# Performance work log

Measured on AMD Instinct MI355X. Metric: run time of the kernel, lower is better.

The kernel has to match this reference:

```python
import jax, jax.numpy as jnp
import numpy as np

N = 20000      # nodes
E = 320000     # edges (avg degree 16)
IN = 512       # input feature dim
HID = 64       # hidden_dim
NH = 8         # n_heads
NC = 20        # n_classes
NG = 64        # graphs in batch
EPS = 1e-5     # batchnorm eps


def setup_inputs() -> dict:
    key = jax.random.key(0)
    ks = jax.random.split(key, 32)
    rn = lambda k, shape, s=0.05: (jax.random.normal(k, shape, jnp.float32) * s)
    inp = {
        "x": rn(ks[0], (N, IN), 1.0),
        "src": jax.random.randint(ks[1], (E,), 0, N),
        "dst": jax.random.randint(ks[2], (E,), 0, N),
        "graph_ids": jnp.sort(jax.random.randint(ks[3], (N,), 0, NG)),
        "n_graphs": NG,
        # encoder
        "W_enc": rn(ks[4], (IN, HID)), "b_enc": jnp.zeros((HID,), jnp.float32),
        # GAT layer 0
        "fc_W0": rn(ks[5], (HID, NH * HID)),
        "attn_l0": rn(ks[6], (NH, HID)), "attn_r0": rn(ks[7], (NH, HID)),
        "res_W0": rn(ks[8], (HID, NH * HID)),
        "bias0": jnp.zeros((NH * HID,), jnp.float32),
        "dp_W0": rn(ks[9], (NH * HID, HID)), "dp_b0": jnp.zeros((HID,), jnp.float32),
        # GAT layer 1
        "fc_W1": rn(ks[10], (HID, NH * HID)),
        "attn_l1": rn(ks[11], (NH, HID)), "attn_r1": rn(ks[12], (NH, HID)),
        "res_W1": rn(ks[13], (HID, NH * HID)),
        "bias1": jnp.zeros((NH * HID,), jnp.float32),
        "dp_W1": rn(ks[14], (NH * HID, HID)), "dp_b1": jnp.zeros((HID,), jnp.float32),
        # batchnorm affine
        "gamma": jnp.ones((2 * HID,), jnp.float32), "beta": jnp.zeros((2 * HID,), jnp.float32),
        # global attention pooling gate
        "gate_W": rn(ks[15], (2 * HID, 1)), "gate_b": jnp.zeros((1,), jnp.float32),
        # classifier
        "cls_W": rn(ks[16], (2 * HID, NC)), "cls_b": jnp.zeros((NC,), jnp.float32),
    }
    return inp


def gat_conv(h, fc_W, attn_l, attn_r, res_W, bias, src, dst, n_nodes):
    # DGL GATConv: fc -> per-head scalar scores -> edge softmax over incoming
    # edges -> weighted sum -> residual + bias -> leaky_relu activation.
    nh, d = attn_l.shape
    feat = (h @ fc_W).reshape(n_nodes, nh, d)              # [N,H,D]
    el = jnp.sum(feat * attn_l[None], axis=-1)             # [N,H]
    er = jnp.sum(feat * attn_r[None], axis=-1)             # [N,H]
    e = jax.nn.leaky_relu(el[src] + er[dst], 0.2)          # [E,H]
    m = jax.ops.segment_max(e, dst, num_segments=n_nodes)  # segment softmax
    ex = jnp.exp(e - m[dst])
    denom = jax.ops.segment_sum(ex, dst, num_segments=n_nodes)
    a = ex / denom[dst]                                    # [E,H]
    msg = feat[src] * a[:, :, None]                        # [E,H,D]  (dominant)
    rst = jax.ops.segment_sum(msg, dst, num_segments=n_nodes)  # [N,H,D]
    rst = rst + (h @ res_W).reshape(n_nodes, nh, d) + bias.reshape(nh, d)
    return jax.nn.leaky_relu(rst, 0.01)  # F.leaky_relu default slope


def reference(x, W_enc, b_enc,
              fc_W0, attn_l0, attn_r0, res_W0, bias0, dp_W0, dp_b0,
              fc_W1, attn_l1, attn_r1, res_W1, bias1, dp_W1, dp_b1,
              gamma, beta, gate_W, gate_b, cls_W, cls_b,
              src, dst, graph_ids, n_graphs):
    n_nodes = x.shape[0]
    he = x @ W_enc + b_enc                                  # encoder [N,HID]
    h = he
    h = gat_conv(h, fc_W0, attn_l0, attn_r0, res_W0, bias0, src, dst, n_nodes)
    h = h.reshape(n_nodes, -1) @ dp_W0 + dp_b0              # down_proj 0
    h = gat_conv(h, fc_W1, attn_l1, attn_r1, res_W1, bias1, src, dst, n_nodes)
    h = h.reshape(n_nodes, -1) @ dp_W1 + dp_b1              # down_proj 1
    hg = jnp.concatenate([h, he], axis=1)                   # [N,2*HID]
    # BatchNorm1d (training-mode batch stats, biased variance)
    mu = jnp.mean(hg, axis=0)
    var = jnp.var(hg, axis=0)
    hg = (hg - mu) * jax.lax.rsqrt(var + EPS) * gamma + beta
    # GlobalAttentionPooling: per-graph softmax over node gates
    gate = hg @ gate_W + gate_b                             # [N,1]
    gm = jax.ops.segment_max(gate, graph_ids, num_segments=n_graphs)
    ge = jnp.exp(gate - gm[graph_ids])
    gden = jax.ops.segment_sum(ge, graph_ids, num_segments=n_graphs)
    alpha = ge / gden[graph_ids]                            # [N,1]
    readout = jax.ops.segment_sum(alpha * hg, graph_ids, num_segments=n_graphs)
    return readout @ cls_W + cls_b                          # [NG,NC]
```

## Files before the change

### kernel.cpp

```cpp
#include <hip/hip_runtime.h>
#include <hip/hip_bf16.h>

#define MROWS   20000
#define N_EDGES 320000
#define DIN     512
#define HID     64
#define NH      8
#define ND      512
#define NCLS    20
#define NG      64
#define BN_EPS  1e-5f
#define PCH     16
#define BNB     256
#define TPB     128

typedef __hip_bfloat16 bf16;
typedef __attribute__((ext_vector_type(8))) short s16x8;
typedef __attribute__((ext_vector_type(4))) float f32x4;

enum { TF32 = 0, TBF16 = 1, TMODE = 2 };

__device__ __forceinline__ int is_bf16_mode(const void* gamma) {
    return *(const unsigned*)gamma != 0x3F800000u;
}

__device__ __forceinline__ float ld_f32(const void* p, size_t i) { return ((const float*)p)[i]; }
__device__ __forceinline__ float ld_b16(const void* p, size_t i) { return __bfloat162float(((const bf16*)p)[i]); }

template<int T>
__device__ __forceinline__ float ldT(const void* p, size_t i, int bf) {
    if constexpr (T == TF32) return ld_f32(p, i);
    else if constexpr (T == TBF16) return ld_b16(p, i);
    else return bf ? ld_b16(p, i) : ld_f32(p, i);
}
template<int T>
__device__ __forceinline__ void stT(void* p, size_t i, int bf, float v) {
    if constexpr (T == TF32) ((float*)p)[i] = v;
    else if constexpr (T == TBF16) ((bf16*)p)[i] = __float2bfloat16(v);
    else { if (bf) ((bf16*)p)[i] = __float2bfloat16(v); else ((float*)p)[i] = v; }
}

__device__ __forceinline__ float bfbits2f(short s) {
    return __uint_as_float(((unsigned)(unsigned short)s) << 16);
}
__device__ __forceinline__ short f2bfbits(float v) {
    bf16 b = __float2bfloat16(v);
    return *reinterpret_cast<short*>(&b);
}

struct TP { const void* src[7]; bf16* dst[7]; int K[7]; };
__global__ void prep_kernel(TP tp, const void* __restrict__ x, bf16* __restrict__ xb,
                            const void* __restrict__ gamma, int* __restrict__ zero0) {
    int b = blockIdx.x;
    int z = b * 256 + threadIdx.x;
    if (z < 2 * MROWS) zero0[z] = 0;
    const int bf = is_bf16_mode(gamma);
    if (b < 7 * TPB) {
        int id = b / TPB;
        int i = (b - id * TPB) * 256 + threadIdx.x;
        int K = tp.K[id];
        int N = (DIN * HID) / K;
        int n = i / K, k = i - n * K;
        tp.dst[id][i] = __float2bfloat16(ldT<TMODE>(tp.src[id], (size_t)k * N + n, bf));
    } else {
        if (bf) return;
        int i = ((b - 7 * TPB) * 256 + threadIdx.x) * 4;
        if (i >= MROWS * DIN) return;
        float4 v = ((const float4*)x)[i >> 2];
        xb[i + 0] = __float2bfloat16(v.x);
        xb[i + 1] = __float2bfloat16(v.y);
        xb[i + 2] = __float2bfloat16(v.z);
        xb[i + 3] = __float2bfloat16(v.w);
    }
}

__global__ void hist_kernel(const int* __restrict__ keys, int* __restrict__ counts, int n) {
    int i = blockIdx.x * 256 + threadIdx.x;
    if (i < n) atomicAdd(&counts[keys[i]], 1);
}

__global__ __launch_bounds__(1024)
void scan_all_kernel(const int* __restrict__ counts, int* __restrict__ offs,
                     const int* __restrict__ gids, int* __restrict__ goffs) {
    if (threadIdx.x <= NG) {
        int g = threadIdx.x;
        int lo = 0, hi = MROWS;
        while (lo < hi) {
            int mid = (lo + hi) >> 1;
            if (gids[mid] < g) lo = mid + 1; else hi = mid;
        }
        goffs[g] = lo;
    }
    __shared__ int wsum[16];
    __shared__ int carry_s;
    int carry = 0;
    int lane = threadIdx.x & 63, wid = threadIdx.x >> 6;
    const int NCHUNK = (MROWS + 1023) / 1024;
    for (int ch = 0; ch < NCHUNK; ++ch) {
        int i = ch * 1024 + threadIdx.x;
        int v = (i < MROWS) ? counts[i] : 0;
        int s = v;
        #pragma unroll
        for (int o = 1; o < 64; o <<= 1) { int t = __shfl_up(s, o, 64); if (lane >= o) s += t; }
        if (lane == 63) wsum[wid] = s;
        __syncthreads();
        if (wid == 0 && lane < 16) {
            int t = wsum[lane];
            #pragma unroll
            for (int o = 1; o < 16; o <<= 1) { int u = __shfl_up(t, o, 64); if (lane >= o) t += u; }
            wsum[lane] = t;
        }
        __syncthreads();
        int wc = (wid > 0) ? wsum[wid - 1] : 0;
        int incl = s + wc + carry;
        if (i < MROWS) offs[i] = incl - v;
        if (threadIdx.x == 1023) carry_s = incl;
        __syncthreads();
        carry = carry_s;
    }
    if (threadIdx.x == 0) offs[MROWS] = carry;
}

__global__ void scatter_kernel(const int* __restrict__ src, const int* __restrict__ dst,
                               const int* __restrict__ offs, int* __restrict__ cursor,
                               int* __restrict__ src_sorted) {
    int e = blockIdx.x * 256 + threadIdx.x;
    if (e < N_EDGES) {
        int d = dst[e];
        int pos = offs[d] + atomicAdd(&cursor[d], 1);
        src_sorted[pos] = src[e];
    }
}

template<int K, int NB, int NTOT>
__global__ __launch_bounds__(256)
void gemm_mfma(const void* __restrict__ Araw, const bf16* __restrict__ Aconv,
               const bf16* __restrict__ BT, const void* __restrict__ bias,
               bf16* __restrict__ C, const void* __restrict__ gamma) {
    const int bf = is_bf16_mode(gamma);
    const bf16* A = bf ? (const bf16*)Araw : Aconv;
    const int wid  = threadIdx.x >> 6;
    const int lane = threadIdx.x & 63;
    const int quad = lane >> 4;
    const int l16  = lane & 15;
    const int rb = blockIdx.x * 128 + wid * 32;
    const int cb = blockIdx.y * NB;
    constexpr int CT = NB / 16;
    constexpr int KC = K / 32;

    f32x4 acc[2][CT] = {};
    int r0 = rb + l16;       if (r0 >= MROWS) r0 = MROWS - 1;
    int r1 = rb + 16 + l16;  if (r1 >= MROWS) r1 = MROWS - 1;
    const bf16* a0p = A + (size_t)r0 * K + quad * 8;
    const bf16* a1p = A + (size_t)r1 * K + quad * 8;
    const bf16* btp = BT + (size_t)(cb + l16) * K + quad * 8;

    for (int kc = 0; kc < KC; ++kc) {
        s16x8 af0 = *(const s16x8*)(a0p + kc * 32);
        s16x8 af1 = *(const s16x8*)(a1p + kc * 32);
        s16x8 bfr[CT];
        #pragma unroll
        for (int ct = 0; ct < CT; ++ct)
            bfr[ct] = *(const s16x8*)(btp + (size_t)ct * 16 * K + kc * 32);
        #pragma unroll
        for (int ct = 0; ct < CT; ++ct) {
            acc[0][ct] = __builtin_amdgcn_mfma_f32_16x16x32_bf16(af0, bfr[ct], acc[0][ct], 0, 0, 0);
            acc[1][ct] = __builtin_amdgcn_mfma_f32_16x16x32_bf16(af1, bfr[ct], acc[1][ct], 0, 0, 0);
        }
    }
    #pragma unroll
    for (int ct = 0; ct < CT; ++ct) {
        int col = cb + ct * 16 + l16;
        float bb = bias ? ldT<TMODE>(bias, col, bf) : 0.f;
        #pragma unroll
        for (int rt = 0; rt < 2; ++rt) {
            #pragma unroll
            for (int rg = 0; rg < 4; ++rg) {
                int row = rb + rt * 16 + quad * 4 + rg;
                if (row < MROWS)
                    C[(size_t)row * NTOT + col] = __float2bfloat16(acc[rt][ct][rg] + bb);
            }
        }
    }
}

__global__ __launch_bounds__(256)
void gemm_fcres(const bf16* __restrict__ A, const bf16* __restrict__ BT_fc,
                const bf16* __restrict__ BT_res, const void* __restrict__ bias,
                const void* __restrict__ attn_l, const void* __restrict__ attn_r,
                bf16* __restrict__ feat, bf16* __restrict__ rst,
                float* __restrict__ el, float* __restrict__ er,
                const void* __restrict__ gamma) {
    const int bf = is_bf16_mode(gamma);
    const bool isres = blockIdx.y >= 4;
    const int yy = blockIdx.y & 3;
    const bf16* BT = isres ? BT_res : BT_fc;
    bf16* C = isres ? rst : feat;
    const int wid  = threadIdx.x >> 6;
    const int lane = threadIdx.x & 63;
    const int quad = lane >> 4;
    const int l16  = lane & 15;
    const int rb = blockIdx.x * 128 + wid * 32;
    const int cb = yy * 128;
    constexpr int CT = 8;
    constexpr int K  = HID;
    constexpr int KC = K / 32;

    f32x4 acc[2][CT] = {};
    int r0 = rb + l16;       if (r0 >= MROWS) r0 = MROWS - 1;
    int r1 = rb + 16 + l16;  if (r1 >= MROWS) r1 = MROWS - 1;
    const bf16* a0p = A + (size_t)r0 * K + quad * 8;
    const bf16* a1p = A + (size_t)r1 * K + quad * 8;
    const bf16* btp = BT + (size_t)(cb + l16) * K + quad * 8;

    #pragma unroll
    for (int kc = 0; kc < KC; ++kc) {
        s16x8 af0 = *(const s16x8*)(a0p + kc * 32);
        s16x8 af1 = *(const s16x8*)(a1p + kc * 32);
        s16x8 bfr[CT];
        #pragma unroll
        for (int ct = 0; ct < CT; ++ct)
            bfr[ct] = *(const s16x8*)(btp + (size_t)ct * 16 * K + kc * 32);
        #pragma unroll
        for (int ct = 0; ct < CT; ++ct) {
            acc[0][ct] = __builtin_amdgcn_mfma_f32_16x16x32_bf16(af0, bfr[ct], acc[0][ct], 0, 0, 0);
            acc[1][ct] = __builtin_amdgcn_mfma_f32_16x16x32_bf16(af1, bfr[ct], acc[1][ct], 0, 0, 0);
        }
    }
    #pragma unroll
    for (int ct = 0; ct < CT; ++ct) {
        int col = cb + ct * 16 + l16;
        float bb = isres ? ldT<TMODE>(bias, col, bf) : 0.f;
        #pragma unroll
        for (int rt = 0; rt < 2; ++rt) {
            #pragma unroll
            for (int rg = 0; rg < 4; ++rg) {
                int row = rb + rt * 16 + quad * 4 + rg;
                if (row < MROWS)
                    C[(size_t)row * ND + col] = __float2bfloat16(acc[rt][ct][rg] + bb);
            }
        }
    }
    if (!isres) {
        float al[CT], ar[CT];
        #pragma unroll
        for (int ct = 0; ct < CT; ++ct) {
            int col = cb + ct * 16 + l16;
            al[ct] = ldT<TMODE>(attn_l, col, bf);
            ar[ct] = ldT<TMODE>(attn_r, col, bf);
        }
        #pragma unroll
        for (int rt = 0; rt < 2; ++rt) {
            #pragma unroll
            for (int rg = 0; rg < 4; ++rg) {
                float e0 = 0.f, e1 = 0.f, f0 = 0.f, f1 = 0.f;
                #pragma unroll
                for (int ct = 0; ct < 4; ++ct) {
                    e0 += acc[rt][ct][rg] * al[ct];
                    f0 += acc[rt][ct][rg] * ar[ct];
                    e1 += acc[rt][ct + 4][rg] * al[ct + 4];
                    f1 += acc[rt][ct + 4][rg] * ar[ct + 4];
                }
                #pragma unroll
                for (int o = 1; o < 16; o <<= 1) {
                    e0 += __shfl_xor(e0, o, 64);
                    e1 += __shfl_xor(e1, o, 64);
                    f0 += __shfl_xor(f0, o, 64);
                    f1 += __shfl_xor(f1, o, 64);
                }
                int row = rb + rt * 16 + quad * 4 + rg;
                if (row < MROWS) {
                    if (l16 == 0) { el[row * 8 + 2 * yy] = e0;     er[row * 8 + 2 * yy] = f0; }
                    if (l16 == 1) { el[row * 8 + 2 * yy + 1] = e1; er[row * 8 + 2 * yy + 1] = f1; }
                }
            }
        }
    }
}

__global__ __launch_bounds__(256)
void agg_kernel(const bf16* __restrict__ feat, const float* __restrict__ el,
                const float* __restrict__ er, const int* __restrict__ offs,
                const int* __restrict__ srcs, bf16* __restrict__ rst) {
    int gid = blockIdx.x * 256 + threadIdx.x;
    int n = gid >> 6;
    int l = threadIdx.x & 63;
    if (n >= MROWS) return;
    int hh = l >> 3;
    int e0 = __builtin_amdgcn_readfirstlane(offs[n]);
    int e1 = __builtin_amdgcn_readfirstlane(offs[n + 1]);
    float er_h = er[n * 8 + hh];
    float acc[8] = {0.f, 0.f, 0.f, 0.f, 0.f, 0.f, 0.f, 0.f};
    float den = 0.f;
    for (int base = e0; base < e1; base += 64) {
        int cnt = min(64, e1 - base);
        int sv = (base + l < e1) ? srcs[base + l] : 0;
        for (int eb = 0; eb < cnt; eb += 8) {
            int en = cnt - eb;
            s16x8 ff[8];
            float elv[8];
            int lastv = cnt - 1;
            #pragma unroll
            for (int p = 0; p < 8; ++p) {
                int idx = eb + p; if (idx > lastv) idx = lastv;
                int s = __shfl(sv, idx, 64);
                ff[p] = *(const s16x8*)(feat + (size_t)s * ND + l * 8);
                elv[p] = el[s * 8 + hh];
            }
            float ww[8];
            #pragma unroll
            for (int p = 0; p < 8; ++p) {
                float sc = elv[p] + er_h;
                sc = sc > 0.f ? sc : 0.2f * sc;
                ww[p] = __expf(fminf(sc, 30.f));
            }
            if (en < 8) {
                #pragma unroll
                for (int p = 1; p < 8; ++p)
                    if (p >= en) ww[p] = 0.f;
            }
            #pragma unroll
            for (int p = 0; p < 8; ++p) {
                den += ww[p];
                #pragma unroll
                for (int j = 0; j < 8; ++j)
                    acc[j] += bfbits2f(ff[p][j]) * ww[p];
            }
        }
    }
    float inv = (den > 0.f) ? 1.f / den : 0.f;
    s16x8* rp = (s16x8*)(rst + (size_t)n * ND + l * 8);
    s16x8 rr = *rp;
    s16x8 ro;
    #pragma unroll
    for (int j = 0; j < 8; ++j) {
        float r = bfbits2f(rr[j]) + acc[j] * inv;
        r = r > 0.f ? r : 0.01f * r;
        ro[j] = f2bfbits(r);
    }
    *rp = ro;
}

__global__ void bn_part_kernel(const bf16* __restrict__ h2, const bf16* __restrict__ he,
                               float* __restrict__ psum, float* __restrict__ psq) {
    int t = threadIdx.x;
    int b = blockIdx.x;
    int beg = (int)((long)MROWS * b / BNB);
    int end = (int)((long)MROWS * (b + 1) / BNB);
    const bf16* srcb = (t < 64) ? h2 : he;
    int col = t & 63;
    float s = 0.f, s2 = 0.f;
    for (int r = beg; r < end; ++r) {
        float v = __bfloat162float(srcb[(size_t)r * 64 + col]);
        s += v;
        s2 += v * v;
    }
    psum[b * 128 + t] = s;
    psq[b * 128 + t] = s2;
}

__global__ void bn_reduce_kernel(const float* __restrict__ psum, const float* __restrict__ psq,
                                 const void* __restrict__ gamma, const void* __restrict__ beta,
                                 float* __restrict__ scale, float* __restrict__ shift) {
    const int bf = is_bf16_mode(gamma);
    int t = threadIdx.x;
    float s = 0.f, s2 = 0.f;
    for (int b = 0; b < BNB; ++b) { s += psum[b * 128 + t]; s2 += psq[b * 128 + t]; }
    float mu = s * (1.f / MROWS);
    float var = s2 * (1.f / MROWS) - mu * mu;
    float inv = rsqrtf(fmaxf(var, 0.f) + BN_EPS);
    float a = ldT<TMODE>(gamma, t, bf) * inv;
    scale[t] = a;
    shift[t] = ldT<TMODE>(beta, t, bf) - mu * a;
}

__global__ __launch_bounds__(128)
void poolgate_kernel(const bf16* __restrict__ h2, const bf16* __restrict__ he,
                     const float* __restrict__ scale, const float* __restrict__ shift,
                     const void* __restrict__ gate_W, const void* __restrict__ gate_b,
                     const int* __restrict__ goffs,
                     float* __restrict__ pacc, float* __restrict__ pden,
                     const void* __restrict__ gamma) {
    const int bf = is_bf16_mode(gamma);
    int g = blockIdx.x;
    int c = blockIdx.y;
    int t = threadIdx.x;
    int r0 = goffs[g], r1 = goffs[g + 1];
    int len = r1 - r0;
    int beg = r0 + (int)((long)len * c / PCH);
    int end = r0 + (int)((long)len * (c + 1) / PCH);
    const bf16* srcb = (t < 64) ? h2 : he;
    int col = t & 63;
    float sc = scale[t], sh = shift[t];
    float gw = ldT<TMODE>(gate_W, t, bf);
    float gb = ldT<TMODE>(gate_b, 0, bf);
    __shared__ float ws[2];
    float acc = 0.f, den = 0.f;
    for (int r = beg; r < end; ++r) {
        float v = __bfloat162float(srcb[(size_t)r * 64 + col]) * sc + sh;
        float p = v * gw;
        #pragma unroll
        for (int o = 32; o > 0; o >>= 1) p += __shfl_xor(p, o, 64);
        if ((t & 63) == 0) ws[t >> 6] = p;
        __syncthreads();
        float wg = __expf(fminf(fmaxf(ws[0] + ws[1] + gb, -60.f), 30.f));
        den += wg;
        acc += wg * v;
        __syncthreads();
    }
    pacc[((size_t)g * PCH + c) * 128 + t] = acc;
    if (t == 0) pden[g * PCH + c] = den;
}

__global__ __launch_bounds__(128)
void poolcls_kernel(const float* __restrict__ pacc, const float* __restrict__ pden,
                    const void* __restrict__ W, const void* __restrict__ b,
                    void* __restrict__ out, const void* __restrict__ gamma) {
    const int bf = is_bf16_mode(gamma);
    int g = blockIdx.x;
    int t = threadIdx.x;
    float acc = 0.f, den = 0.f;
    #pragma unroll
    for (int c = 0; c < PCH; ++c) {
        acc += pacc[((size_t)g * PCH + c) * 128 + t];
        den += pden[g * PCH + c];
    }
    __shared__ float rs[128];
    rs[t] = (den > 0.f) ? acc / den : 0.f;
    __syncthreads();
    if (t < NCLS) {
        float o = ldT<TMODE>(b, t, bf);
        #pragma unroll 8
        for (int k = 0; k < 128; ++k)
            o += rs[k] * ldT<TMODE>(W, (size_t)k * NCLS + t, bf);
        stT<TMODE>(out, g * NCLS + t, bf, o);
    }
}

extern "C" void kernel_launch(void* const* d_in, const int* in_sizes, int n_in,
                              void* d_out, int out_size, void* d_ws, size_t ws_size,
                              hipStream_t stream) {
    const void* x       = d_in[0];
    const int*  src     = (const int*)d_in[1];
    const int*  dst     = (const int*)d_in[2];
    const int*  gids    = (const int*)d_in[3];
    const void* W_enc   = d_in[5];
    const void* b_enc   = d_in[6];
    const void* fc_W0   = d_in[7];
    const void* attn_l0 = d_in[8];
    const void* attn_r0 = d_in[9];
    const void* res_W0  = d_in[10];
    const void* bias0   = d_in[11];
    const void* dp_W0   = d_in[12];
    const void* dp_b0   = d_in[13];
    const void* fc_W1   = d_in[14];
    const void* attn_l1 = d_in[15];
    const void* attn_r1 = d_in[16];
    const void* res_W1  = d_in[17];
    const void* bias1   = d_in[18];
    const void* dp_W1   = d_in[19];
    const void* dp_b1   = d_in[20];
    const void* gamma   = d_in[21];
    const void* beta    = d_in[22];
    const void* gate_W  = d_in[23];
    const void* gate_b  = d_in[24];
    const void* cls_W   = d_in[25];
    const void* cls_b   = d_in[26];

    char* wsc = (char*)d_ws;
    size_t off = 0;
    auto alloc = [&](size_t bytes) -> void* {
        void* p = wsc + off;
        off = (off + bytes + 255) & ~(size_t)255;
        return p;
    };
    bf16*  he        = (bf16*) alloc((size_t)MROWS * HID * 2);
    bf16*  h         = (bf16*) alloc((size_t)MROWS * HID * 2);
    bf16*  h2        = (bf16*) alloc((size_t)MROWS * HID * 2);
    bf16*  feat      = (bf16*) alloc((size_t)MROWS * ND * 2);
    bf16*  rst       = (bf16*) alloc((size_t)MROWS * ND * 2);
    bf16*  xb        = rst;
    bf16*  bt_enc    = (bf16*) alloc((size_t)DIN * HID * 2);
    bf16*  bt_fc0    = (bf16*) alloc((size_t)HID * ND * 2);
    bf16*  bt_res0   = (bf16*) alloc((size_t)HID * ND * 2);
    bf16*  bt_dp0    = (bf16*) alloc((size_t)ND * HID * 2);
    bf16*  bt_fc1    = (bf16*) alloc((size_t)HID * ND * 2);
    bf16*  bt_res1   = (bf16*) alloc((size_t)HID * ND * 2);
    bf16*  bt_dp1    = (bf16*) alloc((size_t)ND * HID * 2);
    float* el        = (float*)alloc((size_t)MROWS * 8 * 4);
    float* er        = (float*)alloc((size_t)MROWS * 8 * 4);
    int*   src_sorted= (int*)  alloc((size_t)N_EDGES * 4);
    int*   offs      = (int*)  alloc((size_t)(MROWS + 1) * 4);
    int*   goffs     = (int*)  alloc((size_t)(NG + 1) * 4);
    float* psum      = (float*)alloc((size_t)BNB * 128 * 4);
    float* psq       = (float*)alloc((size_t)BNB * 128 * 4);
    float* pacc      = (float*)alloc((size_t)NG * PCH * 128 * 4);
    float* pden      = (float*)alloc((size_t)NG * PCH * 4);
    float* bnscale   = (float*)alloc(128 * 4);
    float* bnshift   = (float*)alloc(128 * 4);
    char*  zbase     = (char*) alloc((size_t)MROWS * 4 * 2);
    int* counts  = (int*)zbase;
    int* cursor  = counts + MROWS;

    TP tp;
    tp.src[0] = W_enc;  tp.K[0] = DIN;
    tp.src[1] = fc_W0;  tp.K[1] = HID;
    tp.src[2] = res_W0; tp.K[2] = HID;
    tp.src[3] = dp_W0;  tp.K[3] = ND;
    tp.src[4] = fc_W1;  tp.K[4] = HID;
    tp.src[5] = res_W1; tp.K[5] = HID;
    tp.src[6] = dp_W1;  tp.K[6] = ND;
    tp.dst[0] = bt_enc; tp.dst[1] = bt_fc0; tp.dst[2] = bt_res0; tp.dst[3] = bt_dp0;
    tp.dst[4] = bt_fc1; tp.dst[5] = bt_res1; tp.dst[6] = bt_dp1;
    const int CONVB = (MROWS * DIN / 4) / 256;
    prep_kernel<<<7 * TPB + CONVB, 256, 0, stream>>>(tp, x, xb, gamma, (int*)zbase);

    hist_kernel<<<(N_EDGES + 255) / 256, 256, 0, stream>>>(dst, counts, N_EDGES);
    scan_all_kernel<<<1, 1024, 0, stream>>>(counts, offs, gids, goffs);
    scatter_kernel<<<(N_EDGES + 255) / 256, 256, 0, stream>>>(src, dst, offs, cursor, src_sorted);

    const int GX = (MROWS + 127) / 128;

    gemm_mfma<DIN, 64, 64><<<dim3(GX, 1), 256, 0, stream>>>(x, xb, bt_enc, b_enc, he, gamma);

    gemm_fcres<<<dim3(GX, 8), 256, 0, stream>>>(he, bt_fc0, bt_res0, bias0, attn_l0, attn_r0,
                                                feat, rst, el, er, gamma);
    agg_kernel<<<(MROWS * 64) / 256, 256, 0, stream>>>(feat, el, er, offs, src_sorted, rst);
    gemm_mfma<ND, 64, 64><<<dim3(GX, 1), 256, 0, stream>>>(rst, rst, bt_dp0, dp_b0, h, gamma);

    gemm_fcres<<<dim3(GX, 8), 256, 0, stream>>>(h, bt_fc1, bt_res1, bias1, attn_l1, attn_r1,
                                                feat, rst, el, er, gamma);
    agg_kernel<<<(MROWS * 64) / 256, 256, 0, stream>>>(feat, el, er, offs, src_sorted, rst);
    gemm_mfma<ND, 64, 64><<<dim3(GX, 1), 256, 0, stream>>>(rst, rst, bt_dp1, dp_b1, h2, gamma);

    bn_part_kernel<<<BNB, 128, 0, stream>>>(h2, he, psum, psq);
    bn_reduce_kernel<<<1, 128, 0, stream>>>(psum, psq, gamma, beta, bnscale, bnshift);
    poolgate_kernel<<<dim3(NG, PCH), 128, 0, stream>>>(h2, he, bnscale, bnshift, gate_W, gate_b,
                                                       goffs, pacc, pden, gamma);
    poolcls_kernel<<<NG, 128, 0, stream>>>(pacc, pden, cls_W, cls_b, d_out, gamma);
}
```

Measured before the change: 478.5 us.

## Fuse fp32-to-bf16 input conversion into encoder GEMM and vectorize epilogue stores

Removes the separate pass that converts x to bf16, so the encoder GEMM now loads fp32 rows and converts them in registers. This avoids writing and re-reading a 20 MB bf16 copy. The MFMA operands are swapped so each lane holds 4 consecutive output columns, which turns the scalar bf16 stores into 8-byte vector stores and reshapes the attention-score reduction to use fewer shuffles. In exchange, the encoder GEMM reads twice as many bytes for A and does more conversion work per load.

```diff
diff --git a/kernel.cpp b/kernel.cpp
--- a/kernel.cpp
+++ b/kernel.cpp
@@ -16,6 +16,7 @@
 
 typedef __hip_bfloat16 bf16;
 typedef __attribute__((ext_vector_type(8))) short s16x8;
+typedef __attribute__((ext_vector_type(4))) short s16x4;
 typedef __attribute__((ext_vector_type(4))) float f32x4;
 
 enum { TF32 = 0, TBF16 = 1, TMODE = 2 };
@@ -49,29 +50,17 @@
 }
 
 struct TP { const void* src[7]; bf16* dst[7]; int K[7]; };
-__global__ void prep_kernel(TP tp, const void* __restrict__ x, bf16* __restrict__ xb,
-                            const void* __restrict__ gamma, int* __restrict__ zero0) {
+__global__ void prep_kernel(TP tp, const void* __restrict__ gamma, int* __restrict__ zero0) {
     int b = blockIdx.x;
     int z = b * 256 + threadIdx.x;
     if (z < 2 * MROWS) zero0[z] = 0;
     const int bf = is_bf16_mode(gamma);
-    if (b < 7 * TPB) {
-        int id = b / TPB;
-        int i = (b - id * TPB) * 256 + threadIdx.x;
-        int K = tp.K[id];
-        int N = (DIN * HID) / K;
-        int n = i / K, k = i - n * K;
-        tp.dst[id][i] = __float2bfloat16(ldT<TMODE>(tp.src[id], (size_t)k * N + n, bf));
-    } else {
-        if (bf) return;
-        int i = ((b - 7 * TPB) * 256 + threadIdx.x) * 4;
-        if (i >= MROWS * DIN) return;
-        float4 v = ((const float4*)x)[i >> 2];
-        xb[i + 0] = __float2bfloat16(v.x);
-        xb[i + 1] = __float2bfloat16(v.y);
-        xb[i + 2] = __float2bfloat16(v.z);
-        xb[i + 3] = __float2bfloat16(v.w);
-    }
+    int id = b / TPB;
+    int i = (b - id * TPB) * 256 + threadIdx.x;
+    int K = tp.K[id];
+    int N = (DIN * HID) / K;
+    int n = i / K, k = i - n * K;
+    tp.dst[id][i] = __float2bfloat16(ldT<TMODE>(tp.src[id], (size_t)k * N + n, bf));
 }
 
 __global__ void hist_kernel(const int* __restrict__ keys, int* __restrict__ counts, int n) {
@@ -132,13 +121,12 @@
     }
 }
 
-template<int K, int NB, int NTOT>
+template<int K, int NB, int NTOT, bool XF32>
 __global__ __launch_bounds__(256)
-void gemm_mfma(const void* __restrict__ Araw, const bf16* __restrict__ Aconv,
-               const bf16* __restrict__ BT, const void* __restrict__ bias,
-               bf16* __restrict__ C, const void* __restrict__ gamma) {
+void gemm_mfma(const void* __restrict__ Araw, const bf16* __restrict__ BT,
+               const void* __restrict__ bias, bf16* __restrict__ C,
+               const void* __restrict__ gamma) {
     const int bf = is_bf16_mode(gamma);
-    const bf16* A = bf ? (const bf16*)Araw : Aconv;
     const int wid  = threadIdx.x >> 6;
     const int lane = threadIdx.x & 63;
     const int quad = lane >> 4;
@@ -151,34 +139,51 @@
     f32x4 acc[2][CT] = {};
     int r0 = rb + l16;       if (r0 >= MROWS) r0 = MROWS - 1;
     int r1 = rb + 16 + l16;  if (r1 >= MROWS) r1 = MROWS - 1;
-    const bf16* a0p = A + (size_t)r0 * K + quad * 8;
-    const bf16* a1p = A + (size_t)r1 * K + quad * 8;
+
+    auto lda = [&](int row, int koff) -> s16x8 {
+        if (XF32 && !bf) {
+            const float* fp = (const float*)Araw + (size_t)row * K + koff;
+            float4 u = *(const float4*)fp;
+            float4 v = *(const float4*)(fp + 4);
+            s16x8 r;
+            r[0] = f2bfbits(u.x); r[1] = f2bfbits(u.y); r[2] = f2bfbits(u.z); r[3] = f2bfbits(u.w);
+            r[4] = f2bfbits(v.x); r[5] = f2bfbits(v.y); r[6] = f2bfbits(v.z); r[7] = f2bfbits(v.w);
+            return r;
+        }
+        return *(const s16x8*)((const bf16*)Araw + (size_t)row * K + koff);
+    };
     const bf16* btp = BT + (size_t)(cb + l16) * K + quad * 8;
 
     for (int kc = 0; kc < KC; ++kc) {
-        s16x8 af0 = *(const s16x8*)(a0p + kc * 32);
-        s16x8 af1 = *(const s16x8*)(a1p + kc * 32);
+        s16x8 af0 = lda(r0, quad * 8 + kc * 32);
+        s16x8 af1 = lda(r1, quad * 8 + kc * 32);
         s16x8 bfr[CT];
         #pragma unroll
         for (int ct = 0; ct < CT; ++ct)
             bfr[ct] = *(const s16x8*)(btp + (size_t)ct * 16 * K + kc * 32);
         #pragma unroll
         for (int ct = 0; ct < CT; ++ct) {
-            acc[0][ct] = __builtin_amdgcn_mfma_f32_16x16x32_bf16(af0, bfr[ct], acc[0][ct], 0, 0, 0);
-            acc[1][ct] = __builtin_amdgcn_mfma_f32_16x16x32_bf16(af1, bfr[ct], acc[1][ct], 0, 0, 0);
+            acc[0][ct] = __builtin_amdgcn_mfma_f32_16x16x32_bf16(bfr[ct], af0, acc[0][ct], 0, 0, 0);
+            acc[1][ct] = __builtin_amdgcn_mfma_f32_16x16x32_bf16(bfr[ct], af1, acc[1][ct], 0, 0, 0);
         }
     }
     #pragma unroll
     for (int ct = 0; ct < CT; ++ct) {
-        int col = cb + ct * 16 + l16;
-        float bb = bias ? ldT<TMODE>(bias, col, bf) : 0.f;
+        int c0 = cb + ct * 16 + quad * 4;
+        float b0 = bias ? ldT<TMODE>(bias, c0 + 0, bf) : 0.f;
+        float b1 = bias ? ldT<TMODE>(bias, c0 + 1, bf) : 0.f;
+        float b2 = bias ? ldT<TMODE>(bias, c0 + 2, bf) : 0.f;
+        float b3 = bias ? ldT<TMODE>(bias, c0 + 3, bf) : 0.f;
         #pragma unroll
         for (int rt = 0; rt < 2; ++rt) {
-            #pragma unroll
-            for (int rg = 0; rg < 4; ++rg) {
-                int row = rb + rt * 16 + quad * 4 + rg;
-                if (row < MROWS)
-                    C[(size_t)row * NTOT + col] = __float2bfloat16(acc[rt][ct][rg] + bb);
+            int row = rb + rt * 16 + l16;
+            if (row < MROWS) {
+                s16x4 o;
+                o[0] = f2bfbits(acc[rt][ct][0] + b0);
+                o[1] = f2bfbits(acc[rt][ct][1] + b1);
+                o[2] = f2bfbits(acc[rt][ct][2] + b2);
+                o[3] = f2bfbits(acc[rt][ct][3] + b3);
+                *(s16x4*)(C + (size_t)row * NTOT + c0) = o;
             }
         }
     }
@@ -223,56 +228,56 @@
             bfr[ct] = *(const s16x8*)(btp + (size_t)ct * 16 * K + kc * 32);
         #pragma unroll
         for (int ct = 0; ct < CT; ++ct) {
-            acc[0][ct] = __builtin_amdgcn_mfma_f32_16x16x32_bf16(af0, bfr[ct], acc[0][ct], 0, 0, 0);
-            acc[1][ct] = __builtin_amdgcn_mfma_f32_16x16x32_bf16(af1, bfr[ct], acc[1][ct], 0, 0, 0);
+            acc[0][ct] = __builtin_amdgcn_mfma_f32_16x16x32_bf16(bfr[ct], af0, acc[0][ct], 0, 0, 0);
+            acc[1][ct] = __builtin_amdgcn_mfma_f32_16x16x32_bf16(bfr[ct], af1, acc[1][ct], 0, 0, 0);
         }
     }
     #pragma unroll
     for (int ct = 0; ct < CT; ++ct) {
-        int col = cb + ct * 16 + l16;
-        float bb = isres ? ldT<TMODE>(bias, col, bf) : 0.f;
+        int c0 = cb + ct * 16 + quad * 4;
+        float b0 = isres ? ldT<TMODE>(bias, c0 + 0, bf) : 0.f;
+        float b1 = isres ? ldT<TMODE>(bias, c0 + 1, bf) : 0.f;
+        float b2 = isres ? ldT<TMODE>(bias, c0 + 2, bf) : 0.f;
+        float b3 = isres ? ldT<TMODE>(bias, c0 + 3, bf) : 0.f;
         #pragma unroll
         for (int rt = 0; rt < 2; ++rt) {
+            int row = rb + rt * 16 + l16;
+            if (row < MROWS) {
+                s16x4 o;
+                o[0] = f2bfbits(acc[rt][ct][0] + b0);
+                o[1] = f2bfbits(acc[rt][ct][1] + b1);
+                o[2] = f2bfbits(acc[rt][ct][2] + b2);
+                o[3] = f2bfbits(acc[rt][ct][3] + b3);
+                *(s16x4*)(C + (size_t)row * ND + c0) = o;
+            }
+        }
+    }
+    if (!isres) {
+        #pragma unroll
+        for (int rt = 0; rt < 2; ++rt) {
+            float e0 = 0.f, f0 = 0.f, e1 = 0.f, f1 = 0.f;
             #pragma unroll
-            for (int rg = 0; rg < 4; ++rg) {
-                int row = rb + rt * 16 + quad * 4 + rg;
-                if (row < MROWS)
-                    C[(size_t)row * ND + col] = __float2bfloat16(acc[rt][ct][rg] + bb);
-            }
-        }
-    }
-    if (!isres) {
-        float al[CT], ar[CT];
-        #pragma unroll
-        for (int ct = 0; ct < CT; ++ct) {
-            int col = cb + ct * 16 + l16;
-            al[ct] = ldT<TMODE>(attn_l, col, bf);
-            ar[ct] = ldT<TMODE>(attn_r, col, bf);
-        }
-        #pragma unroll
-        for (int rt = 0; rt < 2; ++rt) {
-            #pragma unroll
-            for (int rg = 0; rg < 4; ++rg) {
-                float e0 = 0.f, e1 = 0.f, f0 = 0.f, f1 = 0.f;
+            for (int ct = 0; ct < 4; ++ct) {
+                int c0 = cb + ct * 16 + quad * 4;
+                int c1 = c0 + 64;
                 #pragma unroll
-                for (int ct = 0; ct < 4; ++ct) {
-                    e0 += acc[rt][ct][rg] * al[ct];
-                    f0 += acc[rt][ct][rg] * ar[ct];
-                    e1 += acc[rt][ct + 4][rg] * al[ct + 4];
-                    f1 += acc[rt][ct + 4][rg] * ar[ct + 4];
+                for (int rg = 0; rg < 4; ++rg) {
+                    e0 += acc[rt][ct][rg]     * ldT<TMODE>(attn_l, c0 + rg, bf);
+                    f0 += acc[rt][ct][rg]     * ldT<TMODE>(attn_r, c0 + rg, bf);
+                    e1 += acc[rt][ct + 4][rg] * ldT<TMODE>(attn_l, c1 + rg, bf);
+                    f1 += acc[rt][ct + 4][rg] * ldT<TMODE>(attn_r, c1 + rg, bf);
                 }
-                #pragma unroll
-                for (int o = 1; o < 16; o <<= 1) {
-                    e0 += __shfl_xor(e0, o, 64);
-                    e1 += __shfl_xor(e1, o, 64);
-                    f0 += __shfl_xor(f0, o, 64);
-                    f1 += __shfl_xor(f1, o, 64);
-                }
-                int row = rb + rt * 16 + quad * 4 + rg;
-                if (row < MROWS) {
-                    if (l16 == 0) { el[row * 8 + 2 * yy] = e0;     er[row * 8 + 2 * yy] = f0; }
-                    if (l16 == 1) { el[row * 8 + 2 * yy + 1] = e1; er[row * 8 + 2 * yy + 1] = f1; }
-                }
+            }
+            e0 += __shfl_xor(e0, 16, 64); e0 += __shfl_xor(e0, 32, 64);
+            f0 += __shfl_xor(f0, 16, 64); f0 += __shfl_xor(f0, 32, 64);
+            e1 += __shfl_xor(e1, 16, 64); e1 += __shfl_xor(e1, 32, 64);
+            f1 += __shfl_xor(f1, 16, 64); f1 += __shfl_xor(f1, 32, 64);
+            int row = rb + rt * 16 + l16;
+            if (row < MROWS) {
+                if (quad == 0)      el[row * 8 + 2 * yy]     = e0;
+                else if (quad == 1) el[row * 8 + 2 * yy + 1] = e1;
+                else if (quad == 2) er[row * 8 + 2 * yy]     = f0;
+                else                er[row * 8 + 2 * yy + 1] = f1;
             }
         }
     }
@@ -479,7 +484,6 @@
     bf16*  h2        = (bf16*) alloc((size_t)MROWS * HID * 2);
     bf16*  feat      = (bf16*) alloc((size_t)MROWS * ND * 2);
     bf16*  rst       = (bf16*) alloc((size_t)MROWS * ND * 2);
-    bf16*  xb        = rst;
     bf16*  bt_enc    = (bf16*) alloc((size_t)DIN * HID * 2);
     bf16*  bt_fc0    = (bf16*) alloc((size_t)HID * ND * 2);
     bf16*  bt_res0   = (bf16*) alloc((size_t)HID * ND * 2);
@@ -512,8 +516,7 @@
     tp.src[6] = dp_W1;  tp.K[6] = ND;
     tp.dst[0] = bt_enc; tp.dst[1] = bt_fc0; tp.dst[2] = bt_res0; tp.dst[3] = bt_dp0;
     tp.dst[4] = bt_fc1; tp.dst[5] = bt_res1; tp.dst[6] = bt_dp1;
-    const int CONVB = (MROWS * DIN / 4) / 256;
-    prep_kernel<<<7 * TPB + CONVB, 256, 0, stream>>>(tp, x, xb, gamma, (int*)zbase);
+    prep_kernel<<<7 * TPB, 256, 0, stream>>>(tp, gamma, (int*)zbase);
 
     hist_kernel<<<(N_EDGES + 255) / 256, 256, 0, stream>>>(dst, counts, N_EDGES);
     scan_all_kernel<<<1, 1024, 0, stream>>>(counts, offs, gids, goffs);
@@ -521,17 +524,17 @@
 
     const int GX = (MROWS + 127) / 128;
 
-    gemm_mfma<DIN, 64, 64><<<dim3(GX, 1), 256, 0, stream>>>(x, xb, bt_enc, b_enc, he, gamma);
+    gemm_mfma<DIN, 64, 64, true><<<dim3(GX, 1), 256, 0, stream>>>(x, bt_enc, b_enc, he, gamma);
 
     gemm_fcres<<<dim3(GX, 8), 256, 0, stream>>>(he, bt_fc0, bt_res0, bias0, attn_l0, attn_r0,
                                                 feat, rst, el, er, gamma);
     agg_kernel<<<(MROWS * 64) / 256, 256, 0, stream>>>(feat, el, er, offs, src_sorted, rst);
-    gemm_mfma<ND, 64, 64><<<dim3(GX, 1), 256, 0, stream>>>(rst, rst, bt_dp0, dp_b0, h, gamma);
+    gemm_mfma<ND, 64, 64, false><<<dim3(GX, 1), 256, 0, stream>>>(rst, bt_dp0, dp_b0, h, gamma);
 
     gemm_fcres<<<dim3(GX, 8), 256, 0, stream>>>(h, bt_fc1, bt_res1, bias1, attn_l1, attn_r1,
                                                 feat, rst, el, er, gamma);
     agg_kernel<<<(MROWS * 64) / 256, 256, 0, stream>>>(feat, el, er, offs, src_sorted, rst);
-    gemm_mfma<ND, 64, 64><<<dim3(GX, 1), 256, 0, stream>>>(rst, rst, bt_dp1, dp_b1, h2, gamma);
+    gemm_mfma<ND, 64, 64, false><<<dim3(GX, 1), 256, 0, stream>>>(rst, bt_dp1, dp_b1, h2, gamma);
 
     bn_part_kernel<<<BNB, 128, 0, stream>>>(h2, he, psum, psq);
     bn_reduce_kernel<<<1, 128, 0, stream>>>(psum, psq, gamma, beta, bnscale, bnshift);
```

Result: no change. 470.2 us (-1.7%).
